# Performance work log

Measured on AMD Instinct MI355X. Metric: run time of the kernel, lower is better.

Reference implementation:

```python
import jax, jax.numpy as jnp
import numpy as np

Z_DIM = 256
N_MOD = 8
CAT = Z_DIM * N_MOD          # 2048
YS = 1024
B = 4096
EPS = 1e-5


def _layer_norm(x, g, b):
    mu = jnp.mean(x, axis=-1, keepdims=True)
    var = jnp.mean((x - mu) ** 2, axis=-1, keepdims=True)
    return (x - mu) * jax.lax.rsqrt(var + EPS) * g + b


def setup_inputs() -> dict:
    key = jax.random.key(0)
    ks = jax.random.split(key, 16)
    s_cat = 1.0 / np.sqrt(CAT)
    s_ys = 1.0 / np.sqrt(YS)
    return {
        "z_stack": jax.random.normal(ks[0], (N_MOD, B, Z_DIM), jnp.float32),
        "Wq": jax.random.normal(ks[1], (CAT, CAT), jnp.float32) * s_cat,
        "bq": jnp.zeros((CAT,), jnp.float32),
        "Wk": jax.random.normal(ks[2], (CAT, CAT), jnp.float32) * s_cat,
        "bk": jnp.zeros((CAT,), jnp.float32),
        "Wv": jax.random.normal(ks[3], (CAT, CAT), jnp.float32) * s_cat,
        "bv": jnp.zeros((CAT,), jnp.float32),
        "W1": jax.random.normal(ks[4], (CAT, YS), jnp.float32) * s_cat,
        "b1": jnp.zeros((YS,), jnp.float32),
        "W2": jax.random.normal(ks[5], (YS, CAT), jnp.float32) * s_ys,
        "b2": jnp.zeros((CAT,), jnp.float32),
        "ln1_g": jnp.ones((CAT,), jnp.float32),
        "ln1_b": jnp.zeros((CAT,), jnp.float32),
        "ln2_g": jnp.ones((CAT,), jnp.float32),
        "ln2_b": jnp.zeros((CAT,), jnp.float32),
        "Wys": jax.random.normal(ks[6], (CAT, YS), jnp.float32) * s_cat,
        "bys": jnp.zeros((YS,), jnp.float32),
        "Ws": jax.random.normal(ks[7], (N_MOD, YS, Z_DIM), jnp.float32) * s_ys,
        "bs": jnp.zeros((N_MOD, Z_DIM), jnp.float32),
    }


def reference(z_stack, Wq, bq, Wk, bk, Wv, bv, W1, b1, W2, b2,
              ln1_g, ln1_b, ln2_g, ln2_b, Wys, bys, Ws, bs):
    M, Bn, Zd = z_stack.shape
    # torch.cat(z, dim=1): [B, M*Zd]
    x = jnp.transpose(z_stack, (1, 0, 2)).reshape(Bn, M * Zd)
    # self-attention over the batch dim (unscaled, as in source)
    q = x @ Wq + bq
    k = x @ Wk + bk
    v = x @ Wv + bv
    attended = jax.nn.softmax(q @ k.T, axis=-1) @ v  # [B, B] scores
    # dropout is identity in eval mode
    x = _layer_norm(x + attended, ln1_g, ln1_b)
    h = jax.nn.gelu(x @ W1 + b1, approximate=False) @ W2 + b2
    h = _layer_norm(x + h, ln2_g, ln2_b)
    yb = h @ Wys + bys                               # [B, YS]
    # per-module scaling layers, stacked output [M, B, Zd]
    y = jnp.einsum('bs,msz->mbz', yb, Ws) + bs[:, None, :]
    return y
```

## Files before the change

kernel.cpp:

```cpp
#include <hip/hip_runtime.h>
#include <hip/hip_bf16.h>
#include <cstdint>
#include <cstddef>
#include <math.h>

typedef __bf16 bf16x8 __attribute__((ext_vector_type(8)));
typedef float  f32x4  __attribute__((ext_vector_type(4)));

#define DEVI __device__ __forceinline__

static constexpr int BB = 4096;
static constexpr int CD = 2048;
static constexpr int ZD = 256;

DEVI unsigned short f2bf(float f) {
  __bf16 h = (__bf16)f;
  return __builtin_bit_cast(unsigned short, h);
}
DEVI float bf2f(unsigned short u) {
  return (float)__builtin_bit_cast(__bf16, u);
}

DEVI void gload_lds16(const void* g, void* l) {
  __builtin_amdgcn_global_load_lds(
      (__attribute__((address_space(1))) void*)(g),
      (__attribute__((address_space(3))) void*)(l), 16, 0, 0);
}

__global__ __launch_bounds__(256) void pack_x(
    const float* __restrict__ z, float* __restrict__ x,
    unsigned short* __restrict__ x2) {
  const int i = (blockIdx.x * 256 + threadIdx.x) * 4;
  const int m  = i >> 20;
  const int r  = i & 1048575;
  const int b  = r >> 8;
  const int zd = r & 255;
  const float4 v = *(const float4*)(z + i);
  const size_t o32 = (size_t)b * CD + m * ZD + zd;
  *(float4*)(x + o32) = v;
  ushort4 h, l;
  h.x = f2bf(v.x); l.x = f2bf(v.x - bf2f(h.x));
  h.y = f2bf(v.y); l.y = f2bf(v.y - bf2f(h.y));
  h.z = f2bf(v.z); l.z = f2bf(v.z - bf2f(h.z));
  h.w = f2bf(v.w); l.w = f2bf(v.w - bf2f(h.w));
  const size_t o2 = (size_t)b * 4096 + m * ZD + zd;
  *(ushort4*)(x2 + o2) = h;
  *(ushort4*)(x2 + o2 + 2048) = l;
}

template<bool LO>
__global__ void transpose_split(const float* __restrict__ in,
                                unsigned short* __restrict__ oh,
                                int R, int C, int ldo) {
  __shared__ float tile[32][33];
  const int c0 = blockIdx.x * 32, r0 = blockIdx.y * 32;
  const int tx = threadIdx.x, ty = threadIdx.y;
#pragma unroll
  for (int k = 0; k < 4; ++k)
    tile[ty + 8 * k][tx] = in[(size_t)(r0 + ty + 8 * k) * C + (c0 + tx)];
  __syncthreads();
#pragma unroll
  for (int k = 0; k < 4; ++k) {
    const float f = tile[tx][ty + 8 * k];
    const size_t o = (size_t)(c0 + ty + 8 * k) * ldo + (r0 + tx);
    const unsigned short h = f2bf(f);
    oh[o] = h;
    if constexpr (LO) oh[o + R] = f2bf(f - bf2f(h));
  }
}

__global__ void transpose_bf16(const unsigned short* __restrict__ in,
                               unsigned short* __restrict__ outp, int R, int C) {
  __shared__ unsigned short tile[32][33];
  const int c0 = blockIdx.x * 32, r0 = blockIdx.y * 32;
  const int tx = threadIdx.x, ty = threadIdx.y;
#pragma unroll
  for (int k = 0; k < 4; ++k)
    tile[ty + 8 * k][tx] = in[(size_t)(r0 + ty + 8 * k) * C + (c0 + tx)];
  __syncthreads();
#pragma unroll
  for (int k = 0; k < 4; ++k)
    outp[(size_t)(c0 + ty + 8 * k) * R + (r0 + tx)] = tile[tx][ty + 8 * k];
}

#define DOMFMA(QI, QJ, AF, BF)                                            \
  {                                                                       \
    _Pragma("unroll") for (int ks = 0; ks < 2; ++ks) {                    \
      _Pragma("unroll") for (int f = 0; f < 4; ++f) {                     \
        _Pragma("unroll") for (int g = 0; g < 2; ++g) {                   \
          acc[(QI) * 4 + f][(QJ) * 2 + g] =                               \
              __builtin_amdgcn_mfma_f32_16x16x32_bf16(                    \
                  AF[f][ks], BF[g][ks], acc[(QI) * 4 + f][(QJ) * 2 + g],  \
                  0, 0, 0);                                               \
        }                                                                 \
      }                                                                   \
    }                                                                     \
  }

#define PH_SYNC()                                         \
  do {                                                    \
    __builtin_amdgcn_s_barrier();                         \
    asm volatile("s_waitcnt lgkmcnt(0)" ::: "memory");    \
    __builtin_amdgcn_sched_barrier(0);                    \
    __builtin_amdgcn_s_setprio(1);                        \
  } while (0)

#define PH_END()                                          \
  do {                                                    \
    __builtin_amdgcn_s_setprio(0);                        \
    __builtin_amdgcn_sched_barrier(0);                    \
    __builtin_amdgcn_s_barrier();                         \
  } while (0)

template<int EP>
__global__ __launch_bounds__(512, 2) void gemm256(
    const unsigned short* __restrict__ A,
    const unsigned short* __restrict__ Bt,
    const float* __restrict__ bq, const float* __restrict__ bk,
    float* __restrict__ Cf,
    unsigned short* __restrict__ Oa, unsigned short* __restrict__ Ob) {
  extern __shared__ char lds[];
  constexpr int NK = 96;
  const int t = threadIdx.x;
  const int lane = t & 63;
  const int w = t >> 6;
  const int wm = w >> 2, wn = w & 3;
  const int lr = lane & 15, kg = lane >> 4;
  const int bid = (blockIdx.x & 7) * 32 + (blockIdx.x >> 3);
  const int bx = bid & 15, by = bid >> 4;
  const int Ar0 = by * 256, Br0 = bx * 256;

  auto stage = [&](const unsigned short* __restrict__ src, int row0, int kk,
                   int dst_off) {
    const int L = t << 4;
    const int Lp = L ^ (((L >> 9) & 1) << 5);
    const int row = Lp >> 7, colb = Lp & 127;
    const char* g = (const char*)src + ((size_t)(row0 + row) * 4096 + kk) * 2 + colb;
    gload_lds16(g, lds + dst_off + ((t >> 6) << 10));
  };
  auto rdA = [&](const char* buf, int qi, int f, int ks) {
    int L = ((qi * 64 + f * 16 + lr) << 7) + ks * 64 + kg * 16;
    L ^= ((L >> 9) & 1) << 5;
    return *(const bf16x8*)(buf + wm * 16384 + L);
  };
  auto rdB = [&](const char* buf, int qj, int g, int ks) {
    int L = ((wn * 64 + qj * 32 + g * 16 + lr) << 7) + ks * 64 + kg * 16;
    L ^= ((L >> 9) & 1) << 5;
    return *(const bf16x8*)(buf + 32768 + L);
  };
  auto kA = [](int k0) { return k0 - ((k0 >> 11) == 2 ? 4096 : 0); };
  auto kB = [](int k0) { return k0 - ((k0 >> 11) >= 1 ? 2048 : 0); };

  f32x4 acc[8][4] = {};
  bf16x8 af[4][2], b0[2][2], b1[2][2];

  {
    stage(A,  Ar0 + 0,   kA(0), 0);
    stage(A,  Ar0 + 64,  kA(0), 8192);
    stage(A,  Ar0 + 128, kA(0), 16384);
    stage(A,  Ar0 + 192, kA(0), 24576);
    stage(Bt, Br0 + 0,   kB(0), 32768);
    stage(Bt, Br0 + 64,  kB(0), 40960);
    stage(Bt, Br0 + 128, kB(0), 49152);
    stage(Bt, Br0 + 192, kB(0), 57344);
    stage(A,  Ar0 + 0,   kA(64), 65536 + 0);
    stage(A,  Ar0 + 128, kA(64), 65536 + 16384);
    stage(Bt, Br0 + 0,   kB(64), 65536 + 32768);
    stage(Bt, Br0 + 64,  kB(64), 65536 + 40960);
    stage(Bt, Br0 + 128, kB(64), 65536 + 49152);
    stage(Bt, Br0 + 192, kB(64), 65536 + 57344);
    asm volatile("s_waitcnt vmcnt(6)" ::: "memory");
    __builtin_amdgcn_sched_barrier(0);
    __builtin_amdgcn_s_barrier();
  }

  for (int tt = 0; tt < NK; ++tt) {
    const int cur = tt & 1;
    const char* buf = lds + cur * 65536;
    const int curo = cur * 65536, nxto = (cur ^ 1) * 65536;
    const int k1 = (tt + 1) * 64, k2 = (tt + 2) * 64;

#pragma unroll
    for (int f = 0; f < 4; ++f)
#pragma unroll
      for (int ks = 0; ks < 2; ++ks) af[f][ks] = rdA(buf, 0, f, ks);
#pragma unroll
    for (int g = 0; g < 2; ++g)
#pragma unroll
      for (int ks = 0; ks < 2; ++ks) b0[g][ks] = rdB(buf, 0, g, ks);
    if (tt + 1 < NK) {
      stage(A, Ar0 + 64,  kA(k1), nxto + 8192);
      stage(A, Ar0 + 192, kA(k1), nxto + 24576);
    }
    PH_SYNC();
    DOMFMA(0, 0, af, b0);
    PH_END();

#pragma unroll
    for (int g = 0; g < 2; ++g)
#pragma unroll
      for (int ks = 0; ks < 2; ++ks) b1[g][ks] = rdB(buf, 1, g, ks);
    if (tt + 2 < NK) {
      stage(A, Ar0 + 0,   kA(k2), curo + 0);
      stage(A, Ar0 + 128, kA(k2), curo + 16384);
    }
    PH_SYNC();
    DOMFMA(0, 1, af, b1);
    PH_END();

#pragma unroll
    for (int f = 0; f < 4; ++f)
#pragma unroll
      for (int ks = 0; ks < 2; ++ks) af[f][ks] = rdA(buf, 1, f, ks);
    if (tt + 2 < NK) {
      stage(Bt, Br0 + 0,  kB(k2), curo + 32768);
      stage(Bt, Br0 + 64, kB(k2), curo + 40960);
    }
    PH_SYNC();
    DOMFMA(1, 0, af, b0);
    PH_END();

    if (tt + 2 < NK) {
      stage(Bt, Br0 + 128, kB(k2), curo + 49152);
      stage(Bt, Br0 + 192, kB(k2), curo + 57344);
      asm volatile("s_waitcnt vmcnt(6)" ::: "memory");
    } else {
      asm volatile("s_waitcnt vmcnt(0)" ::: "memory");
    }
    __builtin_amdgcn_sched_barrier(0);
    PH_SYNC();
    DOMFMA(1, 1, af, b1);
    PH_END();
  }

  const int rbase = Ar0 + wm * 128 + kg * 4;
  const int cbase = Br0 + wn * 64 + lr;
#pragma unroll
  for (int rf = 0; rf < 8; ++rf) {
#pragma unroll
    for (int cf = 0; cf < 4; ++cf) {
      const int col = cbase + cf * 16;
#pragma unroll
      for (int q = 0; q < 4; ++q) {
        const int row = rbase + rf * 16 + q;
        float val = acc[rf][cf][q];
        if constexpr (EP == 0) {
          Cf[(size_t)row * 4096 + col] = val;
        } else {
          if (col < 2048) {
            val += bq[col];
            const unsigned short h = f2bf(val);
            Oa[(size_t)row * 4096 + col] = h;
            Oa[(size_t)row * 4096 + 2048 + col] = f2bf(val - bf2f(h));
          } else {
            const int c2 = col - 2048;
            val += bk[c2];
            const unsigned short h = f2bf(val);
            Ob[(size_t)row * 4096 + c2] = h;
            Ob[(size_t)row * 4096 + 2048 + c2] = f2bf(val - bf2f(h));
          }
        }
      }
    }
  }
}

template<int EP>
__global__ __launch_bounds__(256) void gemm_bt(
    const unsigned short* __restrict__ Ah,
    const unsigned short* __restrict__ Bh,
    const float* __restrict__ bias,
    float* __restrict__ Cf, unsigned short* __restrict__ Cb,
    int M, int N, int K, int lda, int ldb) {
  __shared__ unsigned short lds[2][128 * 32];
  const int t = threadIdx.x;
  const int lane = t & 63;
  const int w = t >> 6;
  const int wr = (w >> 1) * 64, wc = (w & 1) * 64;
  const int lr = lane & 15, kg = lane >> 4;
  const size_t Ar0 = (size_t)blockIdx.y * 128;
  const size_t Br0 = (size_t)blockIdx.x * 128;

  f32x4 acc[4][4] = {};

  for (int k0 = 0; k0 < K; k0 += 32) {
#pragma unroll
    for (int rnd = 0; rnd < 2; ++rnd) {
      const int e = t * 8 + rnd * 2048;
      const int row = e >> 5, col = e & 31;
      const size_t ga = (Ar0 + row) * (size_t)lda + (k0 + col);
      const size_t gb = (Br0 + row) * (size_t)ldb + (k0 + col);
      const int lo = (w << 9) + rnd * 2048;
      gload_lds16(Ah + ga, &lds[0][lo]);
      gload_lds16(Bh + gb, &lds[1][lo]);
    }
    __syncthreads();
    bf16x8 ah[4], bh[4];
#pragma unroll
    for (int i = 0; i < 4; ++i) {
      ah[i] = *(const bf16x8*)&lds[0][((wr + i * 16 + lr) << 5) + (kg << 3)];
      bh[i] = *(const bf16x8*)&lds[1][((wc + i * 16 + lr) << 5) + (kg << 3)];
    }
#pragma unroll
    for (int i = 0; i < 4; ++i)
#pragma unroll
      for (int j = 0; j < 4; ++j)
        acc[i][j] = __builtin_amdgcn_mfma_f32_16x16x32_bf16(ah[i], bh[j], acc[i][j], 0, 0, 0);
    __syncthreads();
  }

  const int rb = (int)Ar0 + wr + (lane >> 4) * 4;
  const int cb = (int)Br0 + wc + lr;
#pragma unroll
  for (int i = 0; i < 4; ++i) {
#pragma unroll
    for (int j = 0; j < 4; ++j) {
      const int col = cb + j * 16;
      const float bsv = bias ? bias[col] : 0.0f;
#pragma unroll
      for (int q = 0; q < 4; ++q) {
        const int row = rb + i * 16 + q;
        const float val = acc[i][j][q] + bsv;
        const size_t o = (size_t)row * N + col;
        if constexpr (EP == 0) {
          Cf[o] = val;
        } else if constexpr (EP == 1) {
          Cb[o] = f2bf(val);
        } else if constexpr (EP == 2) {
          const float ge = 0.5f * val * (1.0f + erff(val * 0.70710678118654752f));
          Cb[o] = f2bf(ge);
        } else {
          const size_t oo = (size_t)(col >> 8) * ((size_t)BB * ZD)
                          + (size_t)row * ZD + (col & 255);
          Cf[oo] = val;
        }
      }
    }
  }
}

__global__ __launch_bounds__(256) void softmax_rows(const float* __restrict__ S,
                                                    unsigned short* __restrict__ P) {
  const int row = blockIdx.x;
  const int t = threadIdx.x;
  const int lane = t & 63, w = t >> 6;
  const float* s = S + (size_t)row * 4096;
  float4 v[4];
  float mx = -3.4e38f;
#pragma unroll
  for (int i = 0; i < 4; ++i) {
    v[i] = *(const float4*)(s + (size_t)(t + 256 * i) * 4);
    mx = fmaxf(mx, fmaxf(fmaxf(v[i].x, v[i].y), fmaxf(v[i].z, v[i].w)));
  }
#pragma unroll
  for (int off = 32; off >= 1; off >>= 1) mx = fmaxf(mx, __shfl_xor(mx, off));
  __shared__ float redm[4], redsum[4];
  if (lane == 0) redm[w] = mx;
  __syncthreads();
  mx = fmaxf(fmaxf(redm[0], redm[1]), fmaxf(redm[2], redm[3]));
  float sum = 0.f;
#pragma unroll
  for (int i = 0; i < 4; ++i) {
    v[i].x = expf(v[i].x - mx);
    v[i].y = expf(v[i].y - mx);
    v[i].z = expf(v[i].z - mx);
    v[i].w = expf(v[i].w - mx);
    sum += v[i].x + v[i].y + v[i].z + v[i].w;
  }
#pragma unroll
  for (int off = 32; off >= 1; off >>= 1) sum += __shfl_xor(sum, off);
  if (lane == 0) redsum[w] = sum;
  __syncthreads();
  sum = redsum[0] + redsum[1] + redsum[2] + redsum[3];
  const float inv = 1.0f / sum;
  unsigned short* p = P + (size_t)row * 4096;
#pragma unroll
  for (int i = 0; i < 4; ++i) {
    ushort4 u;
    u.x = f2bf(v[i].x * inv);
    u.y = f2bf(v[i].y * inv);
    u.z = f2bf(v[i].z * inv);
    u.w = f2bf(v[i].w * inv);
    *(ushort4*)(p + (size_t)(t + 256 * i) * 4) = u;
  }
}

template<bool WF32>
__global__ __launch_bounds__(256) void ln_fused(
    const float* __restrict__ a, const float* __restrict__ b,
    const float* __restrict__ g, const float* __restrict__ be,
    float* __restrict__ of, unsigned short* __restrict__ ob) {
  const int row = blockIdx.x;
  const int t = threadIdx.x;
  const int lane = t & 63, w = t >> 6;
  const float* ar = a + (size_t)row * 2048;
  const float* br = b + (size_t)row * 2048;
  float4 x[2];
  float s = 0.f, ss = 0.f;
#pragma unroll
  for (int i = 0; i < 2; ++i) {
    const int o = (t + 256 * i) * 4;
    const float4 av = *(const float4*)(ar + o);
    const float4 bv = *(const float4*)(br + o);
    x[i].x = av.x + bv.x; x[i].y = av.y + bv.y;
    x[i].z = av.z + bv.z; x[i].w = av.w + bv.w;
    s  += x[i].x + x[i].y + x[i].z + x[i].w;
    ss += x[i].x * x[i].x + x[i].y * x[i].y + x[i].z * x[i].z + x[i].w * x[i].w;
  }
#pragma unroll
  for (int off = 32; off >= 1; off >>= 1) {
    s  += __shfl_xor(s, off);
    ss += __shfl_xor(ss, off);
  }
  __shared__ float rs[4], rss[4];
  if (lane == 0) { rs[w] = s; rss[w] = ss; }
  __syncthreads();
  s  = rs[0] + rs[1] + rs[2] + rs[3];
  ss = rss[0] + rss[1] + rss[2] + rss[3];
  const float mu  = s * (1.0f / 2048.0f);
  const float var = ss * (1.0f / 2048.0f) - mu * mu;
  const float inv = rsqrtf(var + 1e-5f);
#pragma unroll
  for (int i = 0; i < 2; ++i) {
    const int o = (t + 256 * i) * 4;
    const float4 gv  = *(const float4*)(g + o);
    const float4 bev = *(const float4*)(be + o);
    float4 y;
    y.x = (x[i].x - mu) * inv * gv.x + bev.x;
    y.y = (x[i].y - mu) * inv * gv.y + bev.y;
    y.z = (x[i].z - mu) * inv * gv.z + bev.z;
    y.w = (x[i].w - mu) * inv * gv.w + bev.w;
    if constexpr (WF32) *(float4*)(of + (size_t)row * 2048 + o) = y;
    ushort4 u;
    u.x = f2bf(y.x); u.y = f2bf(y.y); u.z = f2bf(y.z); u.w = f2bf(y.w);
    *(ushort4*)(ob + (size_t)row * 2048 + o) = u;
  }
}

extern "C" void kernel_launch(void* const* d_in, const int* in_sizes, int n_in,
                              void* d_out, int out_size, void* d_ws, size_t ws_size,
                              hipStream_t stream) {
  (void)in_sizes; (void)n_in; (void)out_size;
  const float* z    = (const float*)d_in[0];
  const float* Wq   = (const float*)d_in[1];
  const float* bq   = (const float*)d_in[2];
  const float* Wk   = (const float*)d_in[3];
  const float* bk   = (const float*)d_in[4];
  const float* Wv   = (const float*)d_in[5];
  const float* bv   = (const float*)d_in[6];
  const float* W1   = (const float*)d_in[7];
  const float* b1   = (const float*)d_in[8];
  const float* W2   = (const float*)d_in[9];
  const float* b2   = (const float*)d_in[10];
  const float* ln1g = (const float*)d_in[11];
  const float* ln1b = (const float*)d_in[12];
  const float* ln2g = (const float*)d_in[13];
  const float* ln2b = (const float*)d_in[14];
  const float* Wys  = (const float*)d_in[15];
  const float* bys  = (const float*)d_in[16];
  const float* Ws   = (const float*)d_in[17];
  const float* bs   = (const float*)d_in[18];
  float* out = (float*)d_out;
  char* ws = (char*)d_ws;

  const size_t MB = 1048576;
  const size_t off_x    = 0;
  const size_t off_h2   = 0;
  const size_t off_x2   = 32 * MB;
  const size_t off_Bqk  = 64 * MB;
  const size_t off_S    = 32 * MB;
  const size_t off_Aq   = 96 * MB;
  const size_t off_P    = 96 * MB;
  const size_t off_x1f  = 96 * MB;
  const size_t off_Btk  = 128 * MB;
  const size_t off_att  = 128 * MB;
  const size_t off_hmid = 128 * MB;
  const size_t off_ybbf = 136 * MB;
  const size_t off_Vbf  = 160 * MB;
  const size_t off_x1bf = 160 * MB;
  const size_t off_Vt   = 176 * MB;
  const size_t off_x2bf = 176 * MB;
  const size_t off_Wvt  = 192 * MB;
  const size_t off_W1t  = 200 * MB;
  const size_t off_W2t  = 204 * MB;
  const size_t off_Wyst = 208 * MB;
  const size_t off_Wst  = 212 * MB;
  if (ws_size < 216 * MB) return;

#define F32P(o) ((float*)(ws + (o)))
#define BFP(o)  ((unsigned short*)(ws + (o)))

  const dim3 tb(32, 8);

  pack_x<<<8192, 256, 0, stream>>>(z, F32P(off_x), BFP(off_x2));
  transpose_split<true ><<<dim3(64, 64), tb, 0, stream>>>(Wq, BFP(off_Bqk), 2048, 2048, 4096);
  transpose_split<true ><<<dim3(64, 64), tb, 0, stream>>>(Wk, BFP(off_Bqk) + (size_t)2048 * 4096, 2048, 2048, 4096);
  transpose_split<false><<<dim3(64, 64), tb, 0, stream>>>(Wv, BFP(off_Wvt), 2048, 2048, 2048);
  transpose_split<false><<<dim3(32, 64), tb, 0, stream>>>(W1, BFP(off_W1t), 2048, 1024, 2048);
  transpose_split<false><<<dim3(64, 32), tb, 0, stream>>>(W2, BFP(off_W2t), 1024, 2048, 1024);
  transpose_split<false><<<dim3(32, 64), tb, 0, stream>>>(Wys, BFP(off_Wyst), 2048, 1024, 2048);
  for (int m = 0; m < 8; ++m)
    transpose_split<false><<<dim3(8, 32), tb, 0, stream>>>(
        Ws + (size_t)m * 262144, BFP(off_Wst) + (size_t)m * 262144, 1024, 256, 1024);

  gemm_bt<1><<<dim3(16, 32), 256, 0, stream>>>(BFP(off_x2), BFP(off_Wvt), bv,
      nullptr, BFP(off_Vbf), 4096, 2048, 2048, 4096, 2048);
  transpose_bf16<<<dim3(64, 128), tb, 0, stream>>>(BFP(off_Vbf), BFP(off_Vt), 4096, 2048);

  gemm256<1><<<256, 512, 131072, stream>>>(BFP(off_x2), BFP(off_Bqk), bq, bk,
      nullptr, BFP(off_Aq), BFP(off_Btk));

  gemm256<0><<<256, 512, 131072, stream>>>(BFP(off_Aq), BFP(off_Btk), nullptr, nullptr,
      F32P(off_S), nullptr, nullptr);

  softmax_rows<<<4096, 256, 0, stream>>>(F32P(off_S), BFP(off_P));
  gemm_bt<0><<<dim3(16, 32), 256, 0, stream>>>(BFP(off_P), BFP(off_Vt), nullptr,
      F32P(off_att), nullptr, 4096, 2048, 4096, 4096, 4096);
  ln_fused<true ><<<4096, 256, 0, stream>>>(F32P(off_x), F32P(off_att), ln1g, ln1b,
      F32P(off_x1f), BFP(off_x1bf));

  gemm_bt<2><<<dim3(8, 32), 256, 0, stream>>>(BFP(off_x1bf), BFP(off_W1t), b1,
      nullptr, BFP(off_hmid), 4096, 1024, 2048, 2048, 2048);
  gemm_bt<0><<<dim3(16, 32), 256, 0, stream>>>(BFP(off_hmid), BFP(off_W2t), b2,
      F32P(off_h2), nullptr, 4096, 2048, 1024, 1024, 1024);
  ln_fused<false><<<4096, 256, 0, stream>>>(F32P(off_x1f), F32P(off_h2), ln2g, ln2b,
      nullptr, BFP(off_x2bf));

  gemm_bt<1><<<dim3(8, 32), 256, 0, stream>>>(BFP(off_x2bf), BFP(off_Wyst), bys,
      nullptr, BFP(off_ybbf), 4096, 1024, 2048, 2048, 2048);
  gemm_bt<4><<<dim3(16, 32), 256, 0, stream>>>(BFP(off_ybbf), BFP(off_Wst), bs,
      out, nullptr, 4096, 2048, 1024, 1024, 1024);
}
```

Before: 832.5 us.

## Generalize 256x256 pipelined GEMM and use it for all matmuls

Parameterizes the hand-pipelined 256x256 MFMA GEMM (K, leading dims, N, tile grid, segmented-K flag) and adds bias, GELU and scatter epilogues. The simpler 128x128 gemm_bt kernel is removed, so the V, PV, MLP and output GEMMs all run on the larger pipelined kernel. The LDS swizzle changes from a single-bit XOR to a 3-bit XOR across 16-byte chunks to reduce bank conflicts. The cost is low block counts (64 or 128 blocks) on the smaller GEMMs, which may leave many compute units idle.

Result: slower. 852.7 us (+2.4%).

```diff
diff --git a/kernel.cpp b/kernel.cpp
--- a/kernel.cpp
+++ b/kernel.cpp
@@ -26,6 +26,8 @@
       (__attribute__((address_space(1))) void*)(g),
       (__attribute__((address_space(3))) void*)(l), 16, 0, 0);
 }
+
+DEVI int swz(int L) { return L ^ (((L >> 7) & 7) << 4); }
 
 __global__ __launch_bounds__(256) void pack_x(
     const float* __restrict__ z, float* __restrict__ x,
@@ -112,63 +114,63 @@
     __builtin_amdgcn_s_barrier();                         \
   } while (0)
 
-template<int EP>
+template<int EP, bool SEG>
 __global__ __launch_bounds__(512, 2) void gemm256(
     const unsigned short* __restrict__ A,
     const unsigned short* __restrict__ Bt,
-    const float* __restrict__ bq, const float* __restrict__ bk,
+    const float* __restrict__ bias, const float* __restrict__ bias2,
     float* __restrict__ Cf,
-    unsigned short* __restrict__ Oa, unsigned short* __restrict__ Ob) {
+    unsigned short* __restrict__ Ob1, unsigned short* __restrict__ Ob2,
+    int Kv, int lda, int ldb, int N, int nbx) {
   extern __shared__ char lds[];
-  constexpr int NK = 96;
+  const int NK = Kv >> 6;
   const int t = threadIdx.x;
   const int lane = t & 63;
   const int w = t >> 6;
   const int wm = w >> 2, wn = w & 3;
   const int lr = lane & 15, kg = lane >> 4;
-  const int bid = (blockIdx.x & 7) * 32 + (blockIdx.x >> 3);
-  const int bx = bid & 15, by = bid >> 4;
+  const int q8 = gridDim.x >> 3;
+  const int bid = (blockIdx.x & 7) * q8 + (blockIdx.x >> 3);
+  const int bx = bid % nbx, by = bid / nbx;
   const int Ar0 = by * 256, Br0 = bx * 256;
 
-  auto stage = [&](const unsigned short* __restrict__ src, int row0, int kk,
-                   int dst_off) {
+  auto stage = [&](const unsigned short* __restrict__ src, int ld, int row0,
+                   int kk, int dst_off) {
     const int L = t << 4;
-    const int Lp = L ^ (((L >> 9) & 1) << 5);
-    const int row = Lp >> 7, colb = Lp & 127;
-    const char* g = (const char*)src + ((size_t)(row0 + row) * 4096 + kk) * 2 + colb;
+    const int Lp = swz(L);
+    const int row = L >> 7, colb = Lp & 127;
+    const char* g = (const char*)src + ((size_t)(row0 + row) * ld + kk) * 2 + colb;
     gload_lds16(g, lds + dst_off + ((t >> 6) << 10));
   };
   auto rdA = [&](const char* buf, int qi, int f, int ks) {
-    int L = ((qi * 64 + f * 16 + lr) << 7) + ks * 64 + kg * 16;
-    L ^= ((L >> 9) & 1) << 5;
+    const int L = swz(((qi * 64 + f * 16 + lr) << 7) + ks * 64 + kg * 16);
     return *(const bf16x8*)(buf + wm * 16384 + L);
   };
   auto rdB = [&](const char* buf, int qj, int g, int ks) {
-    int L = ((wn * 64 + qj * 32 + g * 16 + lr) << 7) + ks * 64 + kg * 16;
-    L ^= ((L >> 9) & 1) << 5;
+    const int L = swz(((wn * 64 + qj * 32 + g * 16 + lr) << 7) + ks * 64 + kg * 16);
     return *(const bf16x8*)(buf + 32768 + L);
   };
-  auto kA = [](int k0) { return k0 - ((k0 >> 11) == 2 ? 4096 : 0); };
-  auto kB = [](int k0) { return k0 - ((k0 >> 11) >= 1 ? 2048 : 0); };
+  auto kA = [](int k0) { return SEG ? (k0 - ((k0 >> 11) == 2 ? 4096 : 0)) : k0; };
+  auto kB = [](int k0) { return SEG ? (k0 - ((k0 >> 11) >= 1 ? 2048 : 0)) : k0; };
 
   f32x4 acc[8][4] = {};
   bf16x8 af[4][2], b0[2][2], b1[2][2];
 
   {
-    stage(A,  Ar0 + 0,   kA(0), 0);
-    stage(A,  Ar0 + 64,  kA(0), 8192);
-    stage(A,  Ar0 + 128, kA(0), 16384);
-    stage(A,  Ar0 + 192, kA(0), 24576);
-    stage(Bt, Br0 + 0,   kB(0), 32768);
-    stage(Bt, Br0 + 64,  kB(0), 40960);
-    stage(Bt, Br0 + 128, kB(0), 49152);
-    stage(Bt, Br0 + 192, kB(0), 57344);
-    stage(A,  Ar0 + 0,   kA(64), 65536 + 0);
-    stage(A,  Ar0 + 128, kA(64), 65536 + 16384);
-    stage(Bt, Br0 + 0,   kB(64), 65536 + 32768);
-    stage(Bt, Br0 + 64,  kB(64), 65536 + 40960);
-    stage(Bt, Br0 + 128, kB(64), 65536 + 49152);
-    stage(Bt, Br0 + 192, kB(64), 65536 + 57344);
+    stage(A,  lda, Ar0 + 0,   kA(0), 0);
+    stage(A,  lda, Ar0 + 64,  kA(0), 8192);
+    stage(A,  lda, Ar0 + 128, kA(0), 16384);
+    stage(A,  lda, Ar0 + 192, kA(0), 24576);
+    stage(Bt, ldb, Br0 + 0,   kB(0), 32768);
+    stage(Bt, ldb, Br0 + 64,  kB(0), 40960);
+    stage(Bt, ldb, Br0 + 128, kB(0), 49152);
+    stage(Bt, ldb, Br0 + 192, kB(0), 57344);
+    stage(A,  lda, Ar0 + 0,   kA(64), 65536 + 0);
+    stage(A,  lda, Ar0 + 128, kA(64), 65536 + 16384);
+    stage(Bt, ldb, Br0 + 0,   kB(64), 65536 + 32768);
+    stage(Bt, ldb, Br0 + 64,  kB(64), 65536 + 40960);
+    stage(Bt, ldb, Br0 + 128, kB(64), 65536 + 49152);
+    stage(Bt, ldb, Br0 + 192, kB(64), 65536 + 57344);
     asm volatile("s_waitcnt vmcnt(6)" ::: "memory");
     __builtin_amdgcn_sched_barrier(0);
     __builtin_amdgcn_s_barrier();
@@ -189,8 +191,8 @@
 #pragma unroll
       for (int ks = 0; ks < 2; ++ks) b0[g][ks] = rdB(buf, 0, g, ks);
     if (tt + 1 < NK) {
-      stage(A, Ar0 + 64,  kA(k1), nxto + 8192);
-      stage(A, Ar0 + 192, kA(k1), nxto + 24576);
+      stage(A, lda, Ar0 + 64,  kA(k1), nxto + 8192);
+      stage(A, lda, Ar0 + 192, kA(k1), nxto + 24576);
     }
     PH_SYNC();
     DOMFMA(0, 0, af, b0);
@@ -201,8 +203,8 @@
 #pragma unroll
       for (int ks = 0; ks < 2; ++ks) b1[g][ks] = rdB(buf, 1, g, ks);
     if (tt + 2 < NK) {
-      stage(A, Ar0 + 0,   kA(k2), curo + 0);
-      stage(A, Ar0 + 128, kA(k2), curo + 16384);
+      stage(A, lda, Ar0 + 0,   kA(k2), curo + 0);
+      stage(A, lda, Ar0 + 128, kA(k2), curo + 16384);
     }
     PH_SYNC();
     DOMFMA(0, 1, af, b1);
@@ -213,16 +215,16 @@
 #pragma unroll
       for (int ks = 0; ks < 2; ++ks) af[f][ks] = rdA(buf, 1, f, ks);
     if (tt + 2 < NK) {
-      stage(Bt, Br0 + 0,  kB(k2), curo + 32768);
-      stage(Bt, Br0 + 64, kB(k2), curo + 40960);
+      stage(Bt, ldb, Br0 + 0,  kB(k2), curo + 32768);
+      stage(Bt, ldb, Br0 + 64, kB(k2), curo + 40960);
     }
     PH_SYNC();
     DOMFMA(1, 0, af, b0);
     PH_END();
 
     if (tt + 2 < NK) {
-      stage(Bt, Br0 + 128, kB(k2), curo + 49152);
-      stage(Bt, Br0 + 192, kB(k2), curo + 57344);
+      stage(Bt, ldb, Br0 + 128, kB(k2), curo + 49152);
+      stage(Bt, ldb, Br0 + 192, kB(k2), curo + 57344);
       asm volatile("s_waitcnt vmcnt(6)" ::: "memory");
     } else {
       asm volatile("s_waitcnt vmcnt(0)" ::: "memory");
@@ -245,91 +247,30 @@
         const int row = rbase + rf * 16 + q;
         float val = acc[rf][cf][q];
         if constexpr (EP == 0) {
-          Cf[(size_t)row * 4096 + col] = val;
-        } else {
+          if (bias) val += bias[col];
+          Cf[(size_t)row * N + col] = val;
+        } else if constexpr (EP == 1) {
           if (col < 2048) {
-            val += bq[col];
+            val += bias[col];
             const unsigned short h = f2bf(val);
-            Oa[(size_t)row * 4096 + col] = h;
-            Oa[(size_t)row * 4096 + 2048 + col] = f2bf(val - bf2f(h));
+            Ob1[(size_t)row * 4096 + col] = h;
+            Ob1[(size_t)row * 4096 + 2048 + col] = f2bf(val - bf2f(h));
           } else {
             const int c2 = col - 2048;
-            val += bk[c2];
+            val += bias2[c2];
             const unsigned short h = f2bf(val);
-            Ob[(size_t)row * 4096 + c2] = h;
-            Ob[(size_t)row * 4096 + 2048 + c2] = f2bf(val - bf2f(h));
+            Ob2[(size_t)row * 4096 + c2] = h;
+            Ob2[(size_t)row * 4096 + 2048 + c2] = f2bf(val - bf2f(h));
           }
-        }
-      }
-    }
-  }
-}
-
-template<int EP>
-__global__ __launch_bounds__(256) void gemm_bt(
-    const unsigned short* __restrict__ Ah,
-    const unsigned short* __restrict__ Bh,
-    const float* __restrict__ bias,
-    float* __restrict__ Cf, unsigned short* __restrict__ Cb,
-    int M, int N, int K, int lda, int ldb) {
-  __shared__ unsigned short lds[2][128 * 32];
-  const int t = threadIdx.x;
-  const int lane = t & 63;
-  const int w = t >> 6;
-  const int wr = (w >> 1) * 64, wc = (w & 1) * 64;
-  const int lr = lane & 15, kg = lane >> 4;
-  const size_t Ar0 = (size_t)blockIdx.y * 128;
-  const size_t Br0 = (size_t)blockIdx.x * 128;
-
-  f32x4 acc[4][4] = {};
-
-  for (int k0 = 0; k0 < K; k0 += 32) {
-#pragma unroll
-    for (int rnd = 0; rnd < 2; ++rnd) {
-      const int e = t * 8 + rnd * 2048;
-      const int row = e >> 5, col = e & 31;
-      const size_t ga = (Ar0 + row) * (size_t)lda + (k0 + col);
-      const size_t gb = (Br0 + row) * (size_t)ldb + (k0 + col);
-      const int lo = (w << 9) + rnd * 2048;
-      gload_lds16(Ah + ga, &lds[0][lo]);
-      gload_lds16(Bh + gb, &lds[1][lo]);
-    }
-    __syncthreads();
-    bf16x8 ah[4], bh[4];
-#pragma unroll
-    for (int i = 0; i < 4; ++i) {
-      ah[i] = *(const bf16x8*)&lds[0][((wr + i * 16 + lr) << 5) + (kg << 3)];
-      bh[i] = *(const bf16x8*)&lds[1][((wc + i * 16 + lr) << 5) + (kg << 3)];
-    }
-#pragma unroll
-    for (int i = 0; i < 4; ++i)
-#pragma unroll
-      for (int j = 0; j < 4; ++j)
-        acc[i][j] = __builtin_amdgcn_mfma_f32_16x16x32_bf16(ah[i], bh[j], acc[i][j], 0, 0, 0);
-    __syncthreads();
-  }
-
-  const int rb = (int)Ar0 + wr + (lane >> 4) * 4;
-  const int cb = (int)Br0 + wc + lr;
-#pragma unroll
-  for (int i = 0; i < 4; ++i) {
-#pragma unroll
-    for (int j = 0; j < 4; ++j) {
-      const int col = cb + j * 16;
-      const float bsv = bias ? bias[col] : 0.0f;
-#pragma unroll
-      for (int q = 0; q < 4; ++q) {
-        const int row = rb + i * 16 + q;
-        const float val = acc[i][j][q] + bsv;
-        const size_t o = (size_t)row * N + col;
-        if constexpr (EP == 0) {
-          Cf[o] = val;
-        } else if constexpr (EP == 1) {
-          Cb[o] = f2bf(val);
         } else if constexpr (EP == 2) {
+          val += bias[col];
+          Ob1[(size_t)row * N + col] = f2bf(val);
+        } else if constexpr (EP == 3) {
+          val += bias[col];
           const float ge = 0.5f * val * (1.0f + erff(val * 0.70710678118654752f));
-          Cb[o] = f2bf(ge);
+          Ob1[(size_t)row * N + col] = f2bf(ge);
         } else {
+          val += bias[col];
           const size_t oo = (size_t)(col >> 8) * ((size_t)BB * ZD)
                           + (size_t)row * ZD + (col & 255);
           Cf[oo] = val;
@@ -491,6 +432,7 @@
 #define BFP(o)  ((unsigned short*)(ws + (o)))
 
   const dim3 tb(32, 8);
+  const int LDSB = 131072;
 
   pack_x<<<8192, 256, 0, stream>>>(z, F32P(off_x), BFP(off_x2));
   transpose_split<true ><<<dim3(64, 64), tb, 0, stream>>>(Wq, BFP(off_Bqk), 2048, 2048, 4096);
@@ -503,31 +445,31 @@
     transpose_split<false><<<dim3(8, 32), tb, 0, stream>>>(
         Ws + (size_t)m * 262144, BFP(off_Wst) + (size_t)m * 262144, 1024, 256, 1024);
 
-  gemm_bt<1><<<dim3(16, 32), 256, 0, stream>>>(BFP(off_x2), BFP(off_Wvt), bv,
-      nullptr, BFP(off_Vbf), 4096, 2048, 2048, 4096, 2048);
+  gemm256<2, false><<<128, 512, LDSB, stream>>>(BFP(off_x2), BFP(off_Wvt), bv, nullptr,
+      nullptr, BFP(off_Vbf), nullptr, 2048, 4096, 2048, 2048, 8);
   transpose_bf16<<<dim3(64, 128), tb, 0, stream>>>(BFP(off_Vbf), BFP(off_Vt), 4096, 2048);
 
-  gemm256<1><<<256, 512, 131072, stream>>>(BFP(off_x2), BFP(off_Bqk), bq, bk,
-      nullptr, BFP(off_Aq), BFP(off_Btk));
-
-  gemm256<0><<<256, 512, 131072, stream>>>(BFP(off_Aq), BFP(off_Btk), nullptr, nullptr,
-      F32P(off_S), nullptr, nullptr);
+  gemm256<1, true ><<<256, 512, LDSB, stream>>>(BFP(off_x2), BFP(off_Bqk), bq, bk,
+      nullptr, BFP(off_Aq), BFP(off_Btk), 6144, 4096, 4096, 4096, 16);
+
+  gemm256<0, true ><<<256, 512, LDSB, stream>>>(BFP(off_Aq), BFP(off_Btk), nullptr, nullptr,
+      F32P(off_S), nullptr, nullptr, 6144, 4096, 4096, 4096, 16);
 
   softmax_rows<<<4096, 256, 0, stream>>>(F32P(off_S), BFP(off_P));
-  gemm_bt<0><<<dim3(16, 32), 256, 0, stream>>>(BFP(off_P), BFP(off_Vt), nullptr,
-      F32P(off_att), nullptr, 4096, 2048, 4096, 4096, 4096);
+  gemm256<0, false><<<128, 512, LDSB, stream>>>(BFP(off_P), BFP(off_Vt), nullptr, nullptr,
+      F32P(off_att), nullptr, nullptr, 4096, 4096, 4096, 2048, 8);
   ln_fused<true ><<<4096, 256, 0, stream>>>(F32P(off_x), F32P(off_att), ln1g, ln1b,
       F32P(off_x1f), BFP(off_x1bf));
 
-  gemm_bt<2><<<dim3(8, 32), 256, 0, stream>>>(BFP(off_x1bf), BFP(off_W1t), b1,
-      nullptr, BFP(off_hmid), 4096, 1024, 2048, 2048, 2048);
-  gemm_bt<0><<<dim3(16, 32), 256, 0, stream>>>(BFP(off_hmid), BFP(off_W2t), b2,
-      F32P(off_h2), nullptr, 4096, 2048, 1024, 1024, 1024);
+  gemm256<3, false><<<64, 512, LDSB, stream>>>(BFP(off_x1bf), BFP(off_W1t), b1, nullptr,
+      nullptr, BFP(off_hmid), nullptr, 2048, 2048, 2048, 1024, 4);
+  gemm256<0, false><<<128, 512, LDSB, stream>>>(BFP(off_hmid), BFP(off_W2t), b2, nullptr,
+      F32P(off_h2), nullptr, nullptr, 1024, 1024, 1024, 2048, 8);
   ln_fused<false><<<4096, 256, 0, stream>>>(F32P(off_x1f), F32P(off_h2), ln2g, ln2b,
       nullptr, BFP(off_x2bf));
 
-  gemm_bt<1><<<dim3(8, 32), 256, 0, stream>>>(BFP(off_x2bf), BFP(off_Wyst), bys,
-      nullptr, BFP(off_ybbf), 4096, 1024, 2048, 2048, 2048);
-  gemm_bt<4><<<dim3(16, 32), 256, 0, stream>>>(BFP(off_ybbf), BFP(off_Wst), bs,
-      out, nullptr, 4096, 2048, 1024, 1024, 1024);
-}
+  gemm256<2, false><<<64, 512, LDSB, stream>>>(BFP(off_x2bf), BFP(off_Wyst), bys, nullptr,
+      nullptr, BFP(off_ybbf), nullptr, 2048, 2048, 2048, 1024, 4);
+  gemm256<4, false><<<128, 512, LDSB, stream>>>(BFP(off_ybbf), BFP(off_Wst), bs, nullptr,
+      out, nullptr, nullptr, 1024, 1024, 1024, 2048, 8);
+}
```
